# Optimization experiments

Measured on AMD Instinct MI355X. Metric: run time of the kernel, lower is better.

Reference implementation:

```python
import jax, jax.numpy as jnp
import numpy as np

B, S, H = 4, 4096, 2048


def setup_inputs() -> dict:
    key = jax.random.key(0)
    ks = jax.random.split(key, 20)
    def lin(k, fin, fout):
        # torch nn.Linear default init: U(-1/sqrt(fin), 1/sqrt(fin))
        kw, kb = jax.random.split(k)
        bound = 1.0 / np.sqrt(fin)
        W = jax.random.uniform(kw, (fin, fout), jnp.float32, -bound, bound)
        b = jax.random.uniform(kb, (fout,), jnp.float32, -bound, bound)
        return W, b
    hidden_states = jax.random.normal(ks[0], (B, S, H), jnp.float32)
    access_frequency = jax.random.uniform(ks[1], (B, S), jnp.float32)
    importance_score = jax.random.uniform(ks[2], (B, S), jnp.float32)
    sel_W1, sel_b1 = lin(ks[3], H, H // 4)
    sel_W2, sel_b2 = lin(ks[4], H // 4, 3)
    c1_W, c1_b = lin(ks[5], H, H // 2)
    f1_W, f1_b = lin(ks[6], H // 2, H // 2)
    d1_W, d1_b = lin(ks[7], H // 2, H)
    c2_W, c2_b = lin(ks[8], H, H // 4)
    f2_W, f2_b = lin(ks[9], H // 4, H // 4)
    d2_W, d2_b = lin(ks[10], H // 4, H)
    return dict(hidden_states=hidden_states, access_frequency=access_frequency,
                importance_score=importance_score, sel_W1=sel_W1, sel_b1=sel_b1,
                sel_W2=sel_W2, sel_b2=sel_b2, c1_W=c1_W, c1_b=c1_b, f1_W=f1_W,
                f1_b=f1_b, d1_W=d1_W, d1_b=d1_b, c2_W=c2_W, c2_b=c2_b,
                f2_W=f2_W, f2_b=f2_b, d2_W=d2_W, d2_b=d2_b)


def reference(hidden_states, access_frequency, importance_score,
              sel_W1, sel_b1, sel_W2, sel_b2,
              c1_W, c1_b, f1_W, f1_b, d1_W, d1_b,
              c2_W, c2_b, f2_W, f2_b, d2_W, d2_b):
    x = hidden_states  # [B,S,H]
    Hh = x.shape[-1] // 2
    # strategy selector on frequency/importance-modulated features
    combined = jnp.concatenate(
        [x[..., :Hh] * access_frequency[..., None],
         x[..., Hh:] * importance_score[..., None]], axis=-1)  # [B,S,H]
    hmid = jax.nn.relu(jnp.einsum('bsh,hk->bsk', combined, sel_W1) + sel_b1)
    weights = jax.nn.softmax(jnp.einsum('bsk,kl->bsl', hmid, sel_W2) + sel_b2)
    sel = jnp.argmax(weights, axis=-1)  # [B,S] in {0,1,2}
    # expert paths (computed densely, selected per token)
    out1 = (jax.numpy.einsum('bsh,hc->bsc', x, c1_W) + c1_b)
    out1 = jnp.einsum('bsc,cd->bsd', out1, f1_W) + f1_b
    out1 = jnp.einsum('bsc,ch->bsh', out1, d1_W) + d1_b
    out2 = (jnp.einsum('bsh,hc->bsc', x, c2_W) + c2_b)
    out2 = jnp.einsum('bsc,cd->bsd', out2, f2_W) + f2_b
    out2 = jnp.einsum('bsc,ch->bsh', out2, d2_W) + d2_b
    s = sel[..., None]
    out = jnp.where(s == 0, x, jnp.where(s == 1, out1, out2))
    return out
```

## Files before the change

### kernel.cpp

```cpp
#include <hip/hip_runtime.h>


#define RECHECK_TAU 0.02

typedef __bf16 bf16x8 __attribute__((ext_vector_type(8)));
typedef float  f32x4  __attribute__((ext_vector_type(4)));
typedef unsigned short us;

__device__ __forceinline__ float bf2f(us u) {
  union { unsigned u; float f; } v; v.u = ((unsigned)u) << 16;
  return v.f;
}
__device__ __forceinline__ us f2bf(float f) {
  union { float f; unsigned u; } v; v.f = f;
  unsigned r = v.u + 0x7fffu + ((v.u >> 16) & 1u);
  return (us)(r >> 16);
}
__device__ __forceinline__ float scrub(float v) {
  return (v == v && fabsf(v) < 1e30f) ? v : 0.f;
}
__device__ __forceinline__ void gld_lds16(const void* g, void* l) {
  __builtin_amdgcn_global_load_lds(
      (const __attribute__((address_space(1))) void*)g,
      (__attribute__((address_space(3))) void*)l, 16, 0, 0);
}

template<int MODE, int AIDX>
__global__ __launch_bounds__(256) void gemm_bt(
    const void* __restrict__ Ap, const us* __restrict__ BT,
    const float* __restrict__ bias, void* __restrict__ outp,
    const int* __restrict__ aidx, const int* __restrict__ oidx,
    const int* __restrict__ cntp, int N, int K)
{
  const int cnt = cntp[0];
  const int Mp  = (cnt + 127) & ~127;
  const int bm0 = blockIdx.y * 128;
  if (bm0 >= Mp) return;
  const int bn0 = blockIdx.x * 128;

  __shared__ __align__(16) us As[128 * 64];
  __shared__ __align__(16) us Bs[128 * 64];
  const int tid  = threadIdx.x;
  const int lane = tid & 63;
  const int w    = tid >> 6;
  const int wr   = w >> 1, wc = w & 1;

  const us* gb[4];
  const us* gab[4];
  const float* gaf[4];
  us* la[4]; us* lb[4];
#pragma unroll
  for (int i = 0; i < 4; ++i) {
    const int s = i * 256 + tid, m = s >> 3, cp = s & 7, c = cp ^ (m & 7);
    gb[i] = BT + (size_t)(bn0 + m) * K + c * 8;
    lb[i] = &Bs[s * 8];
    la[i] = &As[s * 8];
    if (AIDX) {
      const int arow = aidx[bm0 + m];
      gaf[i] = (const float*)Ap + (size_t)arow * K + c * 8;
    } else {
      gab[i] = (const us*)Ap + (size_t)(bm0 + m) * K + c * 8;
    }
  }

  f32x4 acc[4][4] = {};

  for (int k0 = 0; k0 < K; k0 += 64) {
#pragma unroll
    for (int i = 0; i < 4; ++i) { gld_lds16(gb[i], lb[i]); gb[i] += 64; }
    if (AIDX) {
#pragma unroll
      for (int i = 0; i < 4; ++i) {
        float4 a0 = *(const float4*)gaf[i];
        float4 a1 = *(const float4*)(gaf[i] + 4);
        gaf[i] += 64;
        union { uint4 v; us u[8]; } t;
        t.u[0] = f2bf(a0.x); t.u[1] = f2bf(a0.y);
        t.u[2] = f2bf(a0.z); t.u[3] = f2bf(a0.w);
        t.u[4] = f2bf(a1.x); t.u[5] = f2bf(a1.y);
        t.u[6] = f2bf(a1.z); t.u[7] = f2bf(a1.w);
        *(uint4*)la[i] = t.v;
      }
    } else {
#pragma unroll
      for (int i = 0; i < 4; ++i) { gld_lds16(gab[i], la[i]); gab[i] += 64; }
    }
    __syncthreads();
#pragma unroll
    for (int kk = 0; kk < 2; ++kk) {
      const int cc = kk * 4 + (lane >> 4);
      bf16x8 af[4], bfr[4];
#pragma unroll
      for (int t = 0; t < 4; ++t) {
        const int m = wr * 64 + t * 16 + (lane & 15);
        const int n = wc * 64 + t * 16 + (lane & 15);
        af[t]  = *(const bf16x8*)&As[(m * 8 + (cc ^ (m & 7))) * 8];
        bfr[t] = *(const bf16x8*)&Bs[(n * 8 + (cc ^ (n & 7))) * 8];
      }
#pragma unroll
      for (int mt = 0; mt < 4; ++mt)
#pragma unroll
        for (int nt = 0; nt < 4; ++nt)
          acc[mt][nt] = __builtin_amdgcn_mfma_f32_16x16x32_bf16(
              af[mt], bfr[nt], acc[mt][nt], 0, 0, 0);
    }
    __syncthreads();
  }

  const int colb = bn0 + wc * 64 + (lane & 15);
  const int rowb = bm0 + wr * 64 + ((lane >> 4) << 2);
  float bv[4];
#pragma unroll
  for (int nt = 0; nt < 4; ++nt) bv[nt] = bias[colb + nt * 16];
#pragma unroll
  for (int mt = 0; mt < 4; ++mt) {
#pragma unroll
    for (int r = 0; r < 4; ++r) {
      const int row = rowb + mt * 16 + r;
      if (MODE == 3) {
        if (row >= cnt) continue;
        const size_t orow = (size_t)oidx[row];
#pragma unroll
        for (int nt = 0; nt < 4; ++nt)
          ((float*)outp)[orow * N + colb + nt * 16] =
              scrub(acc[mt][nt][r] + bv[nt]);
      } else {
#pragma unroll
        for (int nt = 0; nt < 4; ++nt)
          ((us*)outp)[(size_t)row * N + colb + nt * 16] =
              f2bf(scrub(acc[mt][nt][r] + bv[nt]));
      }
    }
  }
}

__global__ __launch_bounds__(256) void sel_fast(
    const float* __restrict__ X, const float* __restrict__ FR,
    const float* __restrict__ IM, const us* __restrict__ BTH,
    const float* __restrict__ bias, float* __restrict__ hmid)
{
  constexpr int K = 2048, N = 512;
  __shared__ __align__(16) us As[128 * 64];
  __shared__ __align__(16) us Bs[128 * 64];
  const int tid  = threadIdx.x;
  const int lane = tid & 63;
  const int w    = tid >> 6;
  const int wr   = w >> 1, wc = w & 1;
  const int bm0  = blockIdx.y * 128;
  const int bn0  = blockIdx.x * 128;

  const us* gb[4]; const float* gx[4]; us* lb[4];
  int sOfs[4], cth[4];
  float fr[4], im[4];
#pragma unroll
  for (int i = 0; i < 4; ++i) {
    const int s = i * 256 + tid, m = s >> 3, cp = s & 7, c = cp ^ (m & 7);
    gb[i] = BTH + (size_t)(bn0 + m) * K + c * 8;
    lb[i] = &Bs[s * 8];
    gx[i] = X + (size_t)(bm0 + m) * K + c * 8;
    sOfs[i] = s * 8;
    cth[i]  = c * 8;
    fr[i] = FR[bm0 + m];
    im[i] = IM[bm0 + m];
  }

  f32x4 acc[4][4] = {};

  for (int k0 = 0; k0 < K; k0 += 64) {
#pragma unroll
    for (int i = 0; i < 4; ++i) { gld_lds16(gb[i], lb[i]); gb[i] += 64; }
#pragma unroll
    for (int i = 0; i < 4; ++i) {
      const float md = (k0 + cth[i] < 1024) ? fr[i] : im[i];
      float4 a0 = *(const float4*)gx[i];
      float4 a1 = *(const float4*)(gx[i] + 4);
      gx[i] += 64;
      float av[8] = {a0.x, a0.y, a0.z, a0.w, a1.x, a1.y, a1.z, a1.w};
      union { uint4 v; us u[8]; } t;
#pragma unroll
      for (int j = 0; j < 8; ++j) t.u[j] = f2bf(av[j] * md);
      *(uint4*)&As[sOfs[i]] = t.v;
    }
    __syncthreads();
#pragma unroll
    for (int kk = 0; kk < 2; ++kk) {
      const int cc = kk * 4 + (lane >> 4);
      bf16x8 af[4], bfr[4];
#pragma unroll
      for (int t = 0; t < 4; ++t) {
        const int m = wr * 64 + t * 16 + (lane & 15);
        const int n = wc * 64 + t * 16 + (lane & 15);
        af[t]  = *(const bf16x8*)&As[(m * 8 + (cc ^ (m & 7))) * 8];
        bfr[t] = *(const bf16x8*)&Bs[(n * 8 + (cc ^ (n & 7))) * 8];
      }
#pragma unroll
      for (int mt = 0; mt < 4; ++mt)
#pragma unroll
        for (int nt = 0; nt < 4; ++nt)
          acc[mt][nt] = __builtin_amdgcn_mfma_f32_16x16x32_bf16(
              af[mt], bfr[nt], acc[mt][nt], 0, 0, 0);
    }
    __syncthreads();
  }

  const int colb = bn0 + wc * 64 + (lane & 15);
  const int rowb = bm0 + wr * 64 + ((lane >> 4) << 2);
  float bv[4];
#pragma unroll
  for (int nt = 0; nt < 4; ++nt) bv[nt] = bias[colb + nt * 16];
#pragma unroll
  for (int mt = 0; mt < 4; ++mt)
#pragma unroll
    for (int r = 0; r < 4; ++r) {
      const int row = rowb + mt * 16 + r;
#pragma unroll
      for (int nt = 0; nt < 4; ++nt)
        hmid[(size_t)row * N + colb + nt * 16] =
            fmaxf(scrub(acc[mt][nt][r] + bv[nt]), 0.f);
    }
}

__global__ __launch_bounds__(256) void sel_precise(
    const float* __restrict__ X, const float* __restrict__ FR,
    const float* __restrict__ IM,
    const us* __restrict__ BTH, const us* __restrict__ BTL,
    const float* __restrict__ bias, float* __restrict__ hmid_r,
    const int* __restrict__ ridx, const int* __restrict__ cntp)
{
  constexpr int K = 2048, N = 512;
  const int cnt = cntp[0];
  const int Mp  = (cnt + 127) & ~127;
  const int bm0 = blockIdx.y * 128;
  if (bm0 >= Mp) return;
  const int bn0 = blockIdx.x * 128;

  __shared__ __align__(16) us AsH[128 * 64];
  __shared__ __align__(16) us AsL[128 * 64];
  __shared__ __align__(16) us BsH[128 * 64];
  __shared__ __align__(16) us BsL[128 * 64];
  const int tid  = threadIdx.x;
  const int lane = tid & 63;
  const int w    = tid >> 6;
  const int wr   = w >> 1, wc = w & 1;

  const us* gbh[4]; const us* gbl[4];
  const float* gx[4];
  us* lbh[4]; us* lbl[4];
  int sOfs[4], cth[4];
  float fr[4], im[4];
#pragma unroll
  for (int i = 0; i < 4; ++i) {
    const int s = i * 256 + tid, m = s >> 3, cp = s & 7, c = cp ^ (m & 7);
    gbh[i] = BTH + (size_t)(bn0 + m) * K + c * 8;
    gbl[i] = BTL + (size_t)(bn0 + m) * K + c * 8;
    lbh[i] = &BsH[s * 8];
    lbl[i] = &BsL[s * 8];
    const int arow = ridx[bm0 + m];
    gx[i]  = X + (size_t)arow * K + c * 8;
    sOfs[i] = s * 8;
    cth[i]  = c * 8;
    fr[i] = FR[arow];
    im[i] = IM[arow];
  }

  f32x4 acc[4][4] = {};

  for (int k0 = 0; k0 < K; k0 += 64) {
#pragma unroll
    for (int i = 0; i < 4; ++i) {
      gld_lds16(gbh[i], lbh[i]); gbh[i] += 64;
      gld_lds16(gbl[i], lbl[i]); gbl[i] += 64;
    }
#pragma unroll
    for (int i = 0; i < 4; ++i) {
      const float md = (k0 + cth[i] < 1024) ? fr[i] : im[i];
      float4 a0 = *(const float4*)gx[i];
      float4 a1 = *(const float4*)(gx[i] + 4);
      gx[i] += 64;
      float av[8] = {a0.x, a0.y, a0.z, a0.w, a1.x, a1.y, a1.z, a1.w};
      union { uint4 v; us u[8]; } hu, lu;
#pragma unroll
      for (int j = 0; j < 8; ++j) {
        float a = av[j] * md;
        us h = f2bf(a);
        hu.u[j] = h;
        lu.u[j] = f2bf(a - bf2f(h));
      }
      *(uint4*)&AsH[sOfs[i]] = hu.v;
      *(uint4*)&AsL[sOfs[i]] = lu.v;
    }
    __syncthreads();
#pragma unroll
    for (int kk = 0; kk < 2; ++kk) {
      const int cc = kk * 4 + (lane >> 4);
      bf16x8 ah[4], al[4], bh[4], bl[4];
#pragma unroll
      for (int t = 0; t < 4; ++t) {
        const int m = wr * 64 + t * 16 + (lane & 15);
        const int n = wc * 64 + t * 16 + (lane & 15);
        const int ai = (m * 8 + (cc ^ (m & 7))) * 8;
        const int bi = (n * 8 + (cc ^ (n & 7))) * 8;
        ah[t] = *(const bf16x8*)&AsH[ai];
        al[t] = *(const bf16x8*)&AsL[ai];
        bh[t] = *(const bf16x8*)&BsH[bi];
        bl[t] = *(const bf16x8*)&BsL[bi];
      }
#pragma unroll
      for (int mt = 0; mt < 4; ++mt)
#pragma unroll
        for (int nt = 0; nt < 4; ++nt) {
          acc[mt][nt] = __builtin_amdgcn_mfma_f32_16x16x32_bf16(
              ah[mt], bh[nt], acc[mt][nt], 0, 0, 0);
          acc[mt][nt] = __builtin_amdgcn_mfma_f32_16x16x32_bf16(
              al[mt], bh[nt], acc[mt][nt], 0, 0, 0);
          acc[mt][nt] = __builtin_amdgcn_mfma_f32_16x16x32_bf16(
              ah[mt], bl[nt], acc[mt][nt], 0, 0, 0);
        }
    }
    __syncthreads();
  }

  const int colb = bn0 + wc * 64 + (lane & 15);
  const int rowb = bm0 + wr * 64 + ((lane >> 4) << 2);
  float bv[4];
#pragma unroll
  for (int nt = 0; nt < 4; ++nt) bv[nt] = bias[colb + nt * 16];
#pragma unroll
  for (int mt = 0; mt < 4; ++mt)
#pragma unroll
    for (int r = 0; r < 4; ++r) {
      const int row = rowb + mt * 16 + r;
#pragma unroll
      for (int nt = 0; nt < 4; ++nt)
        hmid_r[(size_t)row * N + colb + nt * 16] =
            fmaxf(scrub(acc[mt][nt][r] + bv[nt]), 0.f);
    }
}

__global__ __launch_bounds__(256) void logits_gap(
    const float* __restrict__ hmid, const float* __restrict__ W2,
    const float* __restrict__ B2, int* __restrict__ sel,
    int* __restrict__ cntr, int* __restrict__ ridx)
{
  const int lane = threadIdx.x & 63;
  const int wv   = threadIdx.x >> 6;
  const int t    = blockIdx.x * 4 + wv;
  const float* h = hmid + (size_t)t * 512;
  double s0 = 0.0, s1 = 0.0, s2 = 0.0;
#pragma unroll
  for (int j = 0; j < 8; ++j) {
    int e = j * 64 + lane;
    double hv = (double)h[e];
    s0 += hv * (double)W2[e * 3 + 0];
    s1 += hv * (double)W2[e * 3 + 1];
    s2 += hv * (double)W2[e * 3 + 2];
  }
  for (int o = 32; o > 0; o >>= 1) {
    s0 += __shfl_down(s0, o);
    s1 += __shfl_down(s1, o);
    s2 += __shfl_down(s2, o);
  }
  if (lane == 0) {
    s0 += (double)B2[0]; s1 += (double)B2[1]; s2 += (double)B2[2];
    int idx = 0; double b = s0;
    if (s1 > b) { b = s1; idx = 1; }
    if (s2 > b) { b = s2; idx = 2; }
    sel[t] = idx;
    const double mn = fmin(fmin(s0, s1), s2);
    const double second = (s0 + s1 + s2) - b - mn;
    if (b - second < RECHECK_TAU) {
      const int p = atomicAdd(cntr, 1);
      ridx[p] = t;
    }
  }
}

__global__ __launch_bounds__(256) void logits_fix(
    const float* __restrict__ hmid_r, const float* __restrict__ W2,
    const float* __restrict__ B2, const int* __restrict__ cntr,
    const int* __restrict__ ridx, int* __restrict__ sel)
{
  const int lane = threadIdx.x & 63;
  const int wv   = threadIdx.x >> 6;
  const int r    = blockIdx.x * 4 + wv;
  if (r >= cntr[0]) return;
  const float* h = hmid_r + (size_t)r * 512;
  double s0 = 0.0, s1 = 0.0, s2 = 0.0;
#pragma unroll
  for (int j = 0; j < 8; ++j) {
    int e = j * 64 + lane;
    double hv = (double)h[e];
    s0 += hv * (double)W2[e * 3 + 0];
    s1 += hv * (double)W2[e * 3 + 1];
    s2 += hv * (double)W2[e * 3 + 2];
  }
  for (int o = 32; o > 0; o >>= 1) {
    s0 += __shfl_down(s0, o);
    s1 += __shfl_down(s1, o);
    s2 += __shfl_down(s2, o);
  }
  if (lane == 0) {
    s0 += (double)B2[0]; s1 += (double)B2[1]; s2 += (double)B2[2];
    int idx = 0; double b = s0;
    if (s1 > b) { b = s1; idx = 1; }
    if (s2 > b) { idx = 2; }
    sel[ridx[r]] = idx;
  }
}

__global__ __launch_bounds__(256) void compact(
    const int* __restrict__ sel, int* __restrict__ cnt,
    int* __restrict__ idx1, int* __restrict__ idx2)
{
  const int t    = blockIdx.x * 256 + threadIdx.x;
  const int lane = threadIdx.x & 63;
  const int w    = threadIdx.x >> 6;
  const int s    = sel[t];
  const bool f1 = (s == 1), f2 = (s == 2);
  const unsigned long long m1 = __ballot(f1);
  const unsigned long long m2 = __ballot(f2);
  const unsigned long long lt = (1ull << lane) - 1ull;
  const int b1 = __popcll(m1 & lt);
  const int b2 = __popcll(m2 & lt);
  __shared__ int w1[4], w2[4], base1, base2;
  if (lane == 0) { w1[w] = __popcll(m1); w2[w] = __popcll(m2); }
  __syncthreads();
  if (threadIdx.x == 0) {
    base1 = atomicAdd(&cnt[0], w1[0] + w1[1] + w1[2] + w1[3]);
    base2 = atomicAdd(&cnt[1], w2[0] + w2[1] + w2[2] + w2[3]);
  }
  __syncthreads();
  int o1 = base1, o2 = base2;
  for (int i = 0; i < w; ++i) { o1 += w1[i]; o2 += w2[i]; }
  if (f1) idx1[o1 + b1] = t;
  if (f2) idx2[o2 + b2] = t;
}

__global__ __launch_bounds__(128) void pad_idx(
    const int* __restrict__ cnt, int* __restrict__ idx1, int* __restrict__ idx2)
{
  idx1[cnt[0] + threadIdx.x] = 0;
  idx2[cnt[1] + threadIdx.x] = 0;
}

__global__ __launch_bounds__(128) void pad_r(
    const int* __restrict__ cntr, int* __restrict__ ridx)
{
  ridx[cntr[0] + threadIdx.x] = 0;
}

__global__ __launch_bounds__(256) void pass0(
    const float* __restrict__ X, const int* __restrict__ sel,
    float* __restrict__ OUT)
{
  const int t = blockIdx.x;
  if (sel[t] != 0) return;
  const uint4* src = (const uint4*)(X + (size_t)t * 2048);
  uint4* dst = (uint4*)(OUT + (size_t)t * 2048);
  dst[threadIdx.x]       = src[threadIdx.x];
  dst[threadIdx.x + 256] = src[threadIdx.x + 256];
}

__global__ __launch_bounds__(256) void transpose_f2b(
    const float* __restrict__ W, us* __restrict__ WT, int K, int N)
{
  __shared__ float tile[32][33];
  const int tx = threadIdx.x & 31, ty = threadIdx.x >> 5;
  const int n0 = blockIdx.x * 32, k0 = blockIdx.y * 32;
#pragma unroll
  for (int r = 0; r < 4; ++r)
    tile[ty + r * 8][tx] = W[(size_t)(k0 + ty + r * 8) * N + n0 + tx];
  __syncthreads();
#pragma unroll
  for (int r = 0; r < 4; ++r)
    WT[(size_t)(n0 + ty + r * 8) * K + k0 + tx] = f2bf(tile[tx][ty + r * 8]);
}

__global__ __launch_bounds__(256) void transpose_split(
    const float* __restrict__ W, us* __restrict__ WH, us* __restrict__ WL,
    int K, int N)
{
  __shared__ float tile[32][33];
  const int tx = threadIdx.x & 31, ty = threadIdx.x >> 5;
  const int n0 = blockIdx.x * 32, k0 = blockIdx.y * 32;
#pragma unroll
  for (int r = 0; r < 4; ++r)
    tile[ty + r * 8][tx] = W[(size_t)(k0 + ty + r * 8) * N + n0 + tx];
  __syncthreads();
#pragma unroll
  for (int r = 0; r < 4; ++r) {
    float v = tile[tx][ty + r * 8];
    us h = f2bf(v);
    const size_t o = (size_t)(n0 + ty + r * 8) * K + k0 + tx;
    WH[o] = h;
    WL[o] = f2bf(v - bf2f(h));
  }
}

extern "C" void kernel_launch(void* const* d_in, const int* in_sizes, int n_in,
                              void* d_out, int out_size, void* d_ws, size_t ws_size,
                              hipStream_t stream) {
  const float* X   = (const float*)d_in[0];
  const float* FR  = (const float*)d_in[1];
  const float* IM  = (const float*)d_in[2];
  const float* W1  = (const float*)d_in[3];
  const float* B1  = (const float*)d_in[4];
  const float* W2  = (const float*)d_in[5];
  const float* B2  = (const float*)d_in[6];
  const float* C1W = (const float*)d_in[7];
  const float* C1B = (const float*)d_in[8];
  const float* F1W = (const float*)d_in[9];
  const float* F1B = (const float*)d_in[10];
  const float* D1W = (const float*)d_in[11];
  const float* D1B = (const float*)d_in[12];
  const float* C2W = (const float*)d_in[13];
  const float* C2B = (const float*)d_in[14];
  const float* F2W = (const float*)d_in[15];
  const float* F2B = (const float*)d_in[16];
  const float* D2W = (const float*)d_in[17];
  const float* D2B = (const float*)d_in[18];
  float* OUT = (float*)d_out;

  size_t off = 0;
  auto alloc = [&](size_t bytes) -> void* {
    void* p = (char*)d_ws + off;
    off += (bytes + 255) & ~(size_t)255;
    return p;
  };
  us* WT_selH = (us*)alloc(512ull * 2048 * 2);
  us* WT_selL = (us*)alloc(512ull * 2048 * 2);
  us* WT_c1   = (us*)alloc(1024ull * 2048 * 2);
  us* WT_f1   = (us*)alloc(1024ull * 1024 * 2);
  us* WT_d1   = (us*)alloc(2048ull * 1024 * 2);
  us* WT_c2   = (us*)alloc(512ull * 2048 * 2);
  us* WT_f2   = (us*)alloc(512ull * 512 * 2);
  us* WT_d2   = (us*)alloc(2048ull * 512 * 2);
  int* sel    = (int*)alloc(16384ull * 4);
  int* cnt    = (int*)alloc(3 * 4);
  int* idx1   = (int*)alloc((16384ull + 128) * 4);
  int* idx2   = (int*)alloc((16384ull + 128) * 4);
  int* ridx   = (int*)alloc((16384ull + 128) * 4);
  void* R1    = alloc(16384ull * 1024 * 2);
  void* R2    = alloc(16384ull * 1024 * 2);
  if (ws_size < off) return;

  float* hmid   = (float*)R1;
  float* hmid_r = (float*)R2;
  us* t1 = (us*)R1;
  us* u1 = (us*)R1;
  us* t2 = (us*)R2;
  us* u2 = (us*)R2;

  const dim3 blk(256);
  transpose_split<<<dim3(16, 64), blk, 0, stream>>>(W1, WT_selH, WT_selL, 2048, 512);
  transpose_f2b<<<dim3(32, 64), blk, 0, stream>>>(C1W, WT_c1, 2048, 1024);
  transpose_f2b<<<dim3(32, 32), blk, 0, stream>>>(F1W, WT_f1, 1024, 1024);
  transpose_f2b<<<dim3(64, 32), blk, 0, stream>>>(D1W, WT_d1, 1024, 2048);
  transpose_f2b<<<dim3(16, 64), blk, 0, stream>>>(C2W, WT_c2, 2048, 512);
  transpose_f2b<<<dim3(16, 16), blk, 0, stream>>>(F2W, WT_f2, 512, 512);
  transpose_f2b<<<dim3(64, 16), blk, 0, stream>>>(D2W, WT_d2, 512, 2048);

  hipMemsetAsync(cnt, 0, 12, stream);

  sel_fast<<<dim3(4, 128), blk, 0, stream>>>(X, FR, IM, WT_selH, B1, hmid);
  logits_gap<<<dim3(4096), blk, 0, stream>>>(hmid, W2, B2, sel, cnt + 2, ridx);
  pad_r<<<dim3(1), dim3(128), 0, stream>>>(cnt + 2, ridx);

  sel_precise<<<dim3(4, 128), blk, 0, stream>>>(X, FR, IM, WT_selH, WT_selL,
                                                B1, hmid_r, ridx, cnt + 2);
  logits_fix<<<dim3(4096), blk, 0, stream>>>(hmid_r, W2, B2, cnt + 2, ridx, sel);

  compact<<<dim3(64), blk, 0, stream>>>(sel, cnt, idx1, idx2);
  pad_idx<<<dim3(1), dim3(128), 0, stream>>>(cnt, idx1, idx2);

  pass0<<<dim3(16384), blk, 0, stream>>>(X, sel, OUT);

  gemm_bt<0, 1><<<dim3(8, 128), blk, 0, stream>>>(X,  WT_c1, C1B, t1, idx1, nullptr, cnt + 0, 1024, 2048);
  gemm_bt<0, 0><<<dim3(8, 128), blk, 0, stream>>>(t1, WT_f1, F1B, t2, nullptr, nullptr, cnt + 0, 1024, 1024);
  gemm_bt<3, 0><<<dim3(16, 128), blk, 0, stream>>>(t2, WT_d1, D1B, OUT, nullptr, idx1, cnt + 0, 2048, 1024);

  gemm_bt<0, 1><<<dim3(4, 128), blk, 0, stream>>>(X,  WT_c2, C2B, u1, idx2, nullptr, cnt + 1, 512, 2048);
  gemm_bt<0, 0><<<dim3(4, 128), blk, 0, stream>>>(u1, WT_f2, F2B, u2, nullptr, nullptr, cnt + 1, 512, 512);
  gemm_bt<3, 0><<<dim3(16, 128), blk, 0, stream>>>(u2, WT_d2, D2B, OUT, nullptr, idx2, cnt + 1, 2048, 512);
}
```

Measured before the change: 747.5 us.

## Precompute bf16 copies of X once and use async LDS loads in GEMMs

Adds an xprep kernel that converts X to bf16 once, both plain and frequency/importance-modulated, so the selector GEMM and the expert GEMMs can load A tiles with global_load_lds instead of converting fp32 in every tile. sel_fast is replaced by the generic gemm_bt with a new ReLU fp32 output mode. Grid axes are swapped so the M dimension maps to blockIdx.x, and the recheck threshold is tightened, which shrinks the precise recheck set. The cost is an extra 64MB write and a larger workspace.

```diff
diff --git a/kernel.cpp b/kernel.cpp
--- a/kernel.cpp
+++ b/kernel.cpp
@@ -1,7 +1,7 @@
 #include <hip/hip_runtime.h>
 
 
-#define RECHECK_TAU 0.02
+#define RECHECK_TAU 0.008
 
 typedef __bf16 bf16x8 __attribute__((ext_vector_type(8)));
 typedef float  f32x4  __attribute__((ext_vector_type(4)));
@@ -25,18 +25,39 @@
       (__attribute__((address_space(3))) void*)l, 16, 0, 0);
 }
 
+__global__ __launch_bounds__(256) void xprep(
+    const float* __restrict__ X, const float* __restrict__ FR,
+    const float* __restrict__ IM, us* __restrict__ Xb, us* __restrict__ Xm)
+{
+  const int t = blockIdx.x;
+  const int j = threadIdx.x;
+  const float fr = FR[t], im = IM[t];
+  const float md = (j < 128) ? fr : im;
+  const float4* src = (const float4*)(X + (size_t)t * 2048);
+  float4 a0 = src[2 * j], a1 = src[2 * j + 1];
+  float av[8] = {a0.x, a0.y, a0.z, a0.w, a1.x, a1.y, a1.z, a1.w};
+  union { uint4 v; us u[8]; } b, m;
+#pragma unroll
+  for (int k = 0; k < 8; ++k) {
+    b.u[k] = f2bf(av[k]);
+    m.u[k] = f2bf(av[k] * md);
+  }
+  ((uint4*)(Xb + (size_t)t * 2048))[j] = b.v;
+  ((uint4*)(Xm + (size_t)t * 2048))[j] = m.v;
+}
+
 template<int MODE, int AIDX>
 __global__ __launch_bounds__(256) void gemm_bt(
-    const void* __restrict__ Ap, const us* __restrict__ BT,
+    const us* __restrict__ Ap, const us* __restrict__ BT,
     const float* __restrict__ bias, void* __restrict__ outp,
     const int* __restrict__ aidx, const int* __restrict__ oidx,
     const int* __restrict__ cntp, int N, int K)
 {
-  const int cnt = cntp[0];
+  const int cnt = cntp ? cntp[0] : (int)(gridDim.x << 7);
   const int Mp  = (cnt + 127) & ~127;
-  const int bm0 = blockIdx.y * 128;
+  const int bm0 = blockIdx.x * 128;
   if (bm0 >= Mp) return;
-  const int bn0 = blockIdx.x * 128;
+  const int bn0 = blockIdx.y * 128;
 
   __shared__ __align__(16) us As[128 * 64];
   __shared__ __align__(16) us Bs[128 * 64];
@@ -46,8 +67,7 @@
   const int wr   = w >> 1, wc = w & 1;
 
   const us* gb[4];
-  const us* gab[4];
-  const float* gaf[4];
+  const us* ga[4];
   us* la[4]; us* lb[4];
 #pragma unroll
   for (int i = 0; i < 4; ++i) {
@@ -55,12 +75,8 @@
     gb[i] = BT + (size_t)(bn0 + m) * K + c * 8;
     lb[i] = &Bs[s * 8];
     la[i] = &As[s * 8];
-    if (AIDX) {
-      const int arow = aidx[bm0 + m];
-      gaf[i] = (const float*)Ap + (size_t)arow * K + c * 8;
-    } else {
-      gab[i] = (const us*)Ap + (size_t)(bm0 + m) * K + c * 8;
-    }
+    const int arow = AIDX ? aidx[bm0 + m] : (bm0 + m);
+    ga[i] = Ap + (size_t)arow * K + c * 8;
   }
 
   f32x4 acc[4][4] = {};
@@ -68,23 +84,8 @@
   for (int k0 = 0; k0 < K; k0 += 64) {
 #pragma unroll
     for (int i = 0; i < 4; ++i) { gld_lds16(gb[i], lb[i]); gb[i] += 64; }
-    if (AIDX) {
-#pragma unroll
-      for (int i = 0; i < 4; ++i) {
-        float4 a0 = *(const float4*)gaf[i];
-        float4 a1 = *(const float4*)(gaf[i] + 4);
-        gaf[i] += 64;
-        union { uint4 v; us u[8]; } t;
-        t.u[0] = f2bf(a0.x); t.u[1] = f2bf(a0.y);
-        t.u[2] = f2bf(a0.z); t.u[3] = f2bf(a0.w);
-        t.u[4] = f2bf(a1.x); t.u[5] = f2bf(a1.y);
-        t.u[6] = f2bf(a1.z); t.u[7] = f2bf(a1.w);
-        *(uint4*)la[i] = t.v;
-      }
-    } else {
-#pragma unroll
-      for (int i = 0; i < 4; ++i) { gld_lds16(gab[i], la[i]); gab[i] += 64; }
-    }
+#pragma unroll
+    for (int i = 0; i < 4; ++i) { gld_lds16(ga[i], la[i]); ga[i] += 64; }
     __syncthreads();
 #pragma unroll
     for (int kk = 0; kk < 2; ++kk) {
@@ -124,6 +125,11 @@
         for (int nt = 0; nt < 4; ++nt)
           ((float*)outp)[orow * N + colb + nt * 16] =
               scrub(acc[mt][nt][r] + bv[nt]);
+      } else if (MODE == 4) {
+#pragma unroll
+        for (int nt = 0; nt < 4; ++nt)
+          ((float*)outp)[(size_t)row * N + colb + nt * 16] =
+              fmaxf(scrub(acc[mt][nt][r] + bv[nt]), 0.f);
       } else {
 #pragma unroll
         for (int nt = 0; nt < 4; ++nt)
@@ -132,92 +138,6 @@
       }
     }
   }
-}
-
-__global__ __launch_bounds__(256) void sel_fast(
-    const float* __restrict__ X, const float* __restrict__ FR,
-    const float* __restrict__ IM, const us* __restrict__ BTH,
-    const float* __restrict__ bias, float* __restrict__ hmid)
-{
-  constexpr int K = 2048, N = 512;
-  __shared__ __align__(16) us As[128 * 64];
-  __shared__ __align__(16) us Bs[128 * 64];
-  const int tid  = threadIdx.x;
-  const int lane = tid & 63;
-  const int w    = tid >> 6;
-  const int wr   = w >> 1, wc = w & 1;
-  const int bm0  = blockIdx.y * 128;
-  const int bn0  = blockIdx.x * 128;
-
-  const us* gb[4]; const float* gx[4]; us* lb[4];
-  int sOfs[4], cth[4];
-  float fr[4], im[4];
-#pragma unroll
-  for (int i = 0; i < 4; ++i) {
-    const int s = i * 256 + tid, m = s >> 3, cp = s & 7, c = cp ^ (m & 7);
-    gb[i] = BTH + (size_t)(bn0 + m) * K + c * 8;
-    lb[i] = &Bs[s * 8];
-    gx[i] = X + (size_t)(bm0 + m) * K + c * 8;
-    sOfs[i] = s * 8;
-    cth[i]  = c * 8;
-    fr[i] = FR[bm0 + m];
-    im[i] = IM[bm0 + m];
-  }
-
-  f32x4 acc[4][4] = {};
-
-  for (int k0 = 0; k0 < K; k0 += 64) {
-#pragma unroll
-    for (int i = 0; i < 4; ++i) { gld_lds16(gb[i], lb[i]); gb[i] += 64; }
-#pragma unroll
-    for (int i = 0; i < 4; ++i) {
-      const float md = (k0 + cth[i] < 1024) ? fr[i] : im[i];
-      float4 a0 = *(const float4*)gx[i];
-      float4 a1 = *(const float4*)(gx[i] + 4);
-      gx[i] += 64;
-      float av[8] = {a0.x, a0.y, a0.z, a0.w, a1.x, a1.y, a1.z, a1.w};
-      union { uint4 v; us u[8]; } t;
-#pragma unroll
-      for (int j = 0; j < 8; ++j) t.u[j] = f2bf(av[j] * md);
-      *(uint4*)&As[sOfs[i]] = t.v;
-    }
-    __syncthreads();
-#pragma unroll
-    for (int kk = 0; kk < 2; ++kk) {
-      const int cc = kk * 4 + (lane >> 4);
-      bf16x8 af[4], bfr[4];
-#pragma unroll
-      for (int t = 0; t < 4; ++t) {
-        const int m = wr * 64 + t * 16 + (lane & 15);
-        const int n = wc * 64 + t * 16 + (lane & 15);
-        af[t]  = *(const bf16x8*)&As[(m * 8 + (cc ^ (m & 7))) * 8];
-        bfr[t] = *(const bf16x8*)&Bs[(n * 8 + (cc ^ (n & 7))) * 8];
-      }
-#pragma unroll
-      for (int mt = 0; mt < 4; ++mt)
-#pragma unroll
-        for (int nt = 0; nt < 4; ++nt)
-          acc[mt][nt] = __builtin_amdgcn_mfma_f32_16x16x32_bf16(
-              af[mt], bfr[nt], acc[mt][nt], 0, 0, 0);
-    }
-    __syncthreads();
-  }
-
-  const int colb = bn0 + wc * 64 + (lane & 15);
-  const int rowb = bm0 + wr * 64 + ((lane >> 4) << 2);
-  float bv[4];
-#pragma unroll
-  for (int nt = 0; nt < 4; ++nt) bv[nt] = bias[colb + nt * 16];
-#pragma unroll
-  for (int mt = 0; mt < 4; ++mt)
-#pragma unroll
-    for (int r = 0; r < 4; ++r) {
-      const int row = rowb + mt * 16 + r;
-#pragma unroll
-      for (int nt = 0; nt < 4; ++nt)
-        hmid[(size_t)row * N + colb + nt * 16] =
-            fmaxf(scrub(acc[mt][nt][r] + bv[nt]), 0.f);
-    }
 }
 
 __global__ __launch_bounds__(256) void sel_precise(
@@ -230,9 +150,9 @@
   constexpr int K = 2048, N = 512;
   const int cnt = cntp[0];
   const int Mp  = (cnt + 127) & ~127;
-  const int bm0 = blockIdx.y * 128;
+  const int bm0 = blockIdx.x * 128;
   if (bm0 >= Mp) return;
-  const int bn0 = blockIdx.x * 128;
+  const int bn0 = blockIdx.y * 128;
 
   __shared__ __align__(16) us AsH[128 * 64];
   __shared__ __align__(16) us AsL[128 * 64];
@@ -540,10 +460,12 @@
   int* idx1   = (int*)alloc((16384ull + 128) * 4);
   int* idx2   = (int*)alloc((16384ull + 128) * 4);
   int* ridx   = (int*)alloc((16384ull + 128) * 4);
+  us*  Xb     = (us*)alloc(16384ull * 2048 * 2);
   void* R1    = alloc(16384ull * 1024 * 2);
-  void* R2    = alloc(16384ull * 1024 * 2);
+  void* R2    = alloc(16384ull * 2048 * 2);
   if (ws_size < off) return;
 
+  us*    Xm     = (us*)R2;
   float* hmid   = (float*)R1;
   float* hmid_r = (float*)R2;
   us* t1 = (us*)R1;
@@ -562,11 +484,14 @@
 
   hipMemsetAsync(cnt, 0, 12, stream);
 
-  sel_fast<<<dim3(4, 128), blk, 0, stream>>>(X, FR, IM, WT_selH, B1, hmid);
+  xprep<<<dim3(16384), blk, 0, stream>>>(X, FR, IM, Xb, Xm);
+
+  gemm_bt<4, 0><<<dim3(128, 4), blk, 0, stream>>>(
+      Xm, WT_selH, B1, hmid, nullptr, nullptr, nullptr, 512, 2048);
   logits_gap<<<dim3(4096), blk, 0, stream>>>(hmid, W2, B2, sel, cnt + 2, ridx);
   pad_r<<<dim3(1), dim3(128), 0, stream>>>(cnt + 2, ridx);
 
-  sel_precise<<<dim3(4, 128), blk, 0, stream>>>(X, FR, IM, WT_selH, WT_selL,
+  sel_precise<<<dim3(128, 4), blk, 0, stream>>>(X, FR, IM, WT_selH, WT_selL,
                                                 B1, hmid_r, ridx, cnt + 2);
   logits_fix<<<dim3(4096), blk, 0, stream>>>(hmid_r, W2, B2, cnt + 2, ridx, sel);
 
@@ -575,11 +500,11 @@
 
   pass0<<<dim3(16384), blk, 0, stream>>>(X, sel, OUT);
 
-  gemm_bt<0, 1><<<dim3(8, 128), blk, 0, stream>>>(X,  WT_c1, C1B, t1, idx1, nullptr, cnt + 0, 1024, 2048);
-  gemm_bt<0, 0><<<dim3(8, 128), blk, 0, stream>>>(t1, WT_f1, F1B, t2, nullptr, nullptr, cnt + 0, 1024, 1024);
-  gemm_bt<3, 0><<<dim3(16, 128), blk, 0, stream>>>(t2, WT_d1, D1B, OUT, nullptr, idx1, cnt + 0, 2048, 1024);
-
-  gemm_bt<0, 1><<<dim3(4, 128), blk, 0, stream>>>(X,  WT_c2, C2B, u1, idx2, nullptr, cnt + 1, 512, 2048);
-  gemm_bt<0, 0><<<dim3(4, 128), blk, 0, stream>>>(u1, WT_f2, F2B, u2, nullptr, nullptr, cnt + 1, 512, 512);
-  gemm_bt<3, 0><<<dim3(16, 128), blk, 0, stream>>>(u2, WT_d2, D2B, OUT, nullptr, idx2, cnt + 1, 2048, 512);
-}
+  gemm_bt<0, 1><<<dim3(128, 8), blk, 0, stream>>>(Xb, WT_c1, C1B, t1, idx1, nullptr, cnt + 0, 1024, 2048);
+  gemm_bt<0, 0><<<dim3(128, 8), blk, 0, stream>>>(t1, WT_f1, F1B, t2, nullptr, nullptr, cnt + 0, 1024, 1024);
+  gemm_bt<3, 0><<<dim3(128, 16), blk, 0, stream>>>(t2, WT_d1, D1B, OUT, nullptr, idx1, cnt + 0, 2048, 1024);
+
+  gemm_bt<0, 1><<<dim3(128, 4), blk, 0, stream>>>(Xb, WT_c2, C2B, u1, idx2, nullptr, cnt + 1, 512, 2048);
+  gemm_bt<0, 0><<<dim3(128, 4), blk, 0, stream>>>(u1, WT_f2, F2B, u2, nullptr, nullptr, cnt + 1, 512, 512);
+  gemm_bt<3, 0><<<dim3(128, 16), blk, 0, stream>>>(u2, WT_d2, D2B, OUT, nullptr, idx2, cnt + 1, 2048, 512);
+}
```

Result: faster. 716.3 us (-4.2%).
